# Kernel optimization log

Measured on AMD Instinct MI355X. Metric: run time of the kernel, lower is better.

## Reference

```python
import jax, jax.numpy as jnp
import numpy as np

CODE_SIZE = 1024
CODE_DIM = 256
B, H, W = 64, 32, 32

def setup_inputs() -> dict:
    key = jax.random.key(0)
    k1, k2 = jax.random.split(key)
    x = jax.random.normal(k1, (B, CODE_DIM, H, W), dtype=jnp.float32)
    # nn.Embedding weight initialized uniform(-1/code_size, 1/code_size)
    weight = jax.random.uniform(k2, (CODE_SIZE, CODE_DIM), dtype=jnp.float32,
                                minval=-1.0 / CODE_SIZE, maxval=1.0 / CODE_SIZE)
    return {"x": x, "weight": weight}

def reference(x, weight):
    b, c, h, w = x.shape
    # (B,C,H,W) -> (B*H*W, C)
    flat = jnp.transpose(x, (0, 2, 3, 1)).reshape(-1, c)
    # squared euclidean distances; argmin of d^2 equals argmin of cdist(p=2)
    d2 = (jnp.sum(flat * flat, axis=1, keepdims=True)
          - 2.0 * (flat @ weight.T)
          + jnp.sum(weight * weight, axis=1)[None, :])  # (N, code_size)
    idxs = jnp.argmin(d2, axis=1).reshape(b, h, w)       # (B,H,W) int
    quantized = jnp.transpose(weight[idxs], (0, 3, 1, 2))  # (B,C,H,W)
    ste = jax.lax.stop_gradient(quantized - x) + x        # straight-through
    return quantized, ste, idxs
```

## Files before the change

### kernel.cpp

```cpp
#include <hip/hip_runtime.h>
#include <math.h>

typedef float vf4 __attribute__((ext_vector_type(4)));

#define CODE_SIZE 1024
#define CODE_DIM  256
#define BB        64
#define HWSZ      1024
#define NROWS     (BB * HWSZ)
#define QELEMS    (BB * CODE_DIM * HWSZ)

__global__ void k_sumsq_w(const float* __restrict__ w, float* __restrict__ sw) {
#pragma clang fp contract(off)
  const int code = blockIdx.x * blockDim.x + threadIdx.x;
  if (code >= CODE_SIZE) return;
  const float* row = w + (size_t)code * CODE_DIM;
  float halves[2];
  for (int h = 0; h < 2; ++h) {
    const float* p = row + h * 128;
    float r[8];
#pragma unroll
    for (int j = 0; j < 8; ++j) { float v = p[j]; r[j] = v * v; }
    for (int i = 8; i < 128; i += 8) {
#pragma unroll
      for (int j = 0; j < 8; ++j) { float v = p[i + j]; r[j] += v * v; }
    }
    halves[h] = ((r[0] + r[1]) + (r[2] + r[3])) + ((r[4] + r[5]) + (r[6] + r[7]));
  }
  sw[code] = halves[0] + halves[1];
}

__global__ void k_sumsq_x(const float* __restrict__ x, float* __restrict__ sx) {
#pragma clang fp contract(off)
  const int n = blockIdx.x * blockDim.x + threadIdx.x;
  const int b = n >> 10, hw = n & 1023;
  const float* p = x + (size_t)b * CODE_DIM * HWSZ + hw;
  float halves[2];
  for (int h = 0; h < 2; ++h) {
    const float* q = p + (size_t)(h * 128) * HWSZ;
    float r[8];
#pragma unroll
    for (int j = 0; j < 8; ++j) { float v = q[(size_t)j * HWSZ]; r[j] = v * v; }
    for (int i = 8; i < 128; i += 8) {
#pragma unroll
      for (int j = 0; j < 8; ++j) { float v = q[(size_t)(i + j) * HWSZ]; r[j] += v * v; }
    }
    halves[h] = ((r[0] + r[1]) + (r[2] + r[3])) + ((r[4] + r[5]) + (r[6] + r[7]));
  }
  sx[n] = halves[0] + halves[1];
}

#define MT  64
#define NTC 256
#define NCH (CODE_SIZE / NTC)
#define KC  32

__launch_bounds__(256, 4)
__global__ void k_argmin(const float* __restrict__ x, const float* __restrict__ w,
                         const float* __restrict__ sx, const float* __restrict__ sw,
                         float* __restrict__ oidx) {
  __shared__ float xs[KC * MT];
  __shared__ float ws[KC * NTC];

  const int t   = threadIdx.x;
  const int n0  = blockIdx.x * MT;
  const int b   = n0 >> 10;
  const int hw0 = n0 & 1023;
  const int rt  = t & 7;
  const int ct  = t >> 3;

  float bk[8]; float bi[8];
#pragma unroll
  for (int ri = 0; ri < 8; ++ri) { bk[ri] = INFINITY; bi[ri] = (float)CODE_SIZE; }

  for (int chunk = 0; chunk < NCH; ++chunk) {
    const int code0 = chunk * NTC;

    float acc[8][8];
#pragma unroll
    for (int ri = 0; ri < 8; ++ri)
#pragma unroll
      for (int cj = 0; cj < 8; ++cj) acc[ri][cj] = 0.0f;

    for (int kc = 0; kc < CODE_DIM / KC; ++kc) {
      const int kbase = kc * KC;
      __syncthreads();
      {
#pragma unroll
        for (int i = 0; i < 2; ++i) {
          const int j  = t + 256 * i;
          const int k  = j >> 4;
          const int rq = j & 15;
          vf4 v = *(const vf4*)(x + ((size_t)(b * CODE_DIM + kbase + k) * HWSZ + hw0 + rq * 4));
          *(vf4*)(xs + k * MT + rq * 4) = v;
        }
      }
      {
        const float* wr = w + (size_t)(code0 + t) * CODE_DIM + kbase;
#pragma unroll
        for (int q = 0; q < 8; ++q) {
          vf4 v = *(const vf4*)(wr + q * 4);
          ws[(q * 4 + 0) * NTC + t] = v.x;
          ws[(q * 4 + 1) * NTC + t] = v.y;
          ws[(q * 4 + 2) * NTC + t] = v.z;
          ws[(q * 4 + 3) * NTC + t] = v.w;
        }
      }
      __syncthreads();

      const float* xp = xs + rt * 8;
      const float* wp = ws + ct * 8;
#pragma unroll 4
      for (int k = 0; k < KC; ++k) {
        vf4 xv0 = *(const vf4*)(xp + k * MT);
        vf4 xv1 = *(const vf4*)(xp + k * MT + 4);
        vf4 wv0 = *(const vf4*)(wp + k * NTC);
        vf4 wv1 = *(const vf4*)(wp + k * NTC + 4);
        float xr[8] = {xv0.x, xv0.y, xv0.z, xv0.w, xv1.x, xv1.y, xv1.z, xv1.w};
        float wc[8] = {wv0.x, wv0.y, wv0.z, wv0.w, wv1.x, wv1.y, wv1.z, wv1.w};
#pragma unroll
        for (int ri = 0; ri < 8; ++ri)
#pragma unroll
          for (int cj = 0; cj < 8; ++cj)
            acc[ri][cj] = fmaf(xr[ri], wc[cj], acc[ri][cj]);
      }
    }

    {
#pragma clang fp contract(off)
      float sxr[8];
#pragma unroll
      for (int ri = 0; ri < 8; ++ri) sxr[ri] = sx[n0 + rt * 8 + ri];
#pragma unroll
      for (int cj = 0; cj < 8; ++cj) {
        const int code = code0 + ct * 8 + cj;
        const float swv = sw[code];
        const float codef = (float)code;
#pragma unroll
        for (int ri = 0; ri < 8; ++ri) {
          const float tmp = sxr[ri] - 2.0f * acc[ri][cj];
          const float key = tmp + swv;
          if (key < bk[ri] || (key == bk[ri] && codef < bi[ri])) {
            bk[ri] = key; bi[ri] = codef;
          }
        }
      }
    }
  }

  __syncthreads();
  float* redk = ws;
  float* redi = ws + 32 * MT;
#pragma unroll
  for (int ri = 0; ri < 8; ++ri) {
    const int row = rt * 8 + ri;
    redk[ct * MT + row] = bk[ri];
    redi[ct * MT + row] = bi[ri];
  }
  __syncthreads();
  if (t < MT) {
    float k0 = redk[t]; float i0 = redi[t];
    for (int q = 1; q < 32; ++q) {
      const float kq = redk[q * MT + t];
      const float iq = redi[q * MT + t];
      if (kq < k0 || (kq == k0 && iq < i0)) { k0 = kq; i0 = iq; }
    }
    oidx[n0 + t] = i0;
  }
}

#define WT_S 65

__global__ void k_epilogue(const float* __restrict__ x, const float* __restrict__ w,
                           const float* __restrict__ oidx, float* __restrict__ out) {
#pragma clang fp contract(off)
  __shared__ int   idxs[MT];
  __shared__ float wt[CODE_DIM * WT_S];

  const int t   = threadIdx.x;
  const int n0  = blockIdx.x * MT;
  const int b   = n0 >> 10;
  const int hw0 = n0 & 1023;

  if (t < MT) idxs[t] = (int)oidx[n0 + t];
  __syncthreads();

#pragma unroll
  for (int i = 0; i < 16; ++i) {
    const int j  = t + 256 * i;
    const int r  = j & 63;
    const int cq = j >> 6;
    vf4 v = *(const vf4*)(w + (size_t)idxs[r] * CODE_DIM + cq * 4);
    wt[(cq * 4 + 0) * WT_S + r] = v.x;
    wt[(cq * 4 + 1) * WT_S + r] = v.y;
    wt[(cq * 4 + 2) * WT_S + r] = v.z;
    wt[(cq * 4 + 3) * WT_S + r] = v.w;
  }
  __syncthreads();

#pragma unroll
  for (int i = 0; i < 16; ++i) {
    const int j  = t + 256 * i;
    const int c  = j >> 4;
    const int rq = j & 15;
    const size_t off = (size_t)(b * CODE_DIM + c) * HWSZ + hw0 + rq * 4;
    vf4 xv = *(const vf4*)(x + off);
    vf4 q, s;
#pragma unroll
    for (int u = 0; u < 4; ++u) {
      const float qv = wt[c * WT_S + rq * 4 + u];
      q[u] = qv;
      const float d = qv - xv[u];
      s[u] = d + xv[u];
    }
    *(vf4*)(out + off) = q;
    *(vf4*)(out + (size_t)QELEMS + off) = s;
  }
}

extern "C" void kernel_launch(void* const* d_in, const int* in_sizes, int n_in,
                              void* d_out, int out_size, void* d_ws, size_t ws_size,
                              hipStream_t stream) {
  const float* x = (const float*)d_in[0];
  const float* w = (const float*)d_in[1];
  float* out  = (float*)d_out;
  float* oidx = out + 2 * (size_t)QELEMS;
  float* sx = out + (size_t)QELEMS;
  float* sw = out + (size_t)QELEMS + NROWS;

  k_sumsq_w<<<CODE_SIZE / 256, 256, 0, stream>>>(w, sw);
  k_sumsq_x<<<NROWS / 256, 256, 0, stream>>>(x, sx);
  k_argmin<<<NROWS / MT, 256, 0, stream>>>(x, w, sx, sw, oidx);
  k_epilogue<<<NROWS / MT, 256, 0, stream>>>(x, w, oidx, out);
}
```

Measured before the change: 618.1 us.

## Replace LDS-tiled argmin GEMM with per-lane rows and wave-uniform codebook loads

The argmin kernel drops its shared-memory staging of x and codebook tiles and its per-k-chunk barriers. Each lane now owns one spatial row and keeps its x values in registers. Each wave handles a block of 64 codes per chunk, so codebook reads are wave-uniform and can go through scalar loads. The aim is to remove LDS traffic and synchronisation, at the cost of rereading x from global memory in every wave and chunk, keeping 64 accumulators per lane, and relying on scalar-cache bandwidth and latency to feed the FMAs.

```diff
diff --git a/kernel.cpp b/kernel.cpp
--- a/kernel.cpp
+++ b/kernel.cpp
@@ -50,119 +50,81 @@
   sx[n] = halves[0] + halves[1];
 }
 
-#define MT  64
-#define NTC 256
-#define NCH (CODE_SIZE / NTC)
-#define KC  32
+#define MT     64
+#define NCH    4
+#define WCODES 64
+#define KC     16
 
-__launch_bounds__(256, 4)
+__launch_bounds__(256, 3)
 __global__ void k_argmin(const float* __restrict__ x, const float* __restrict__ w,
                          const float* __restrict__ sx, const float* __restrict__ sw,
                          float* __restrict__ oidx) {
-  __shared__ float xs[KC * MT];
-  __shared__ float ws[KC * NTC];
+  __shared__ float redk[4][MT];
+  __shared__ float redi[4][MT];
 
-  const int t   = threadIdx.x;
-  const int n0  = blockIdx.x * MT;
-  const int b   = n0 >> 10;
-  const int hw0 = n0 & 1023;
-  const int rt  = t & 7;
-  const int ct  = t >> 3;
+  const int t    = threadIdx.x;
+  const int lane = t & 63;
+  const int wv   = __builtin_amdgcn_readfirstlane(t >> 6);
+  const int n0   = blockIdx.x * MT;
+  const int b    = n0 >> 10;
+  const int hw0  = n0 & 1023;
 
-  float bk[8]; float bi[8];
-#pragma unroll
-  for (int ri = 0; ri < 8; ++ri) { bk[ri] = INFINITY; bi[ri] = (float)CODE_SIZE; }
+  const float* xlane = x + (size_t)b * CODE_DIM * HWSZ + hw0 + lane;
+  const float  sxr   = sx[n0 + lane];
+
+  float bk = INFINITY, bi = (float)CODE_SIZE;
 
   for (int chunk = 0; chunk < NCH; ++chunk) {
-    const int code0 = chunk * NTC;
+    const int code0 = chunk * (NCH * WCODES) + wv * WCODES;
 
-    float acc[8][8];
+    float acc[WCODES];
 #pragma unroll
-    for (int ri = 0; ri < 8; ++ri)
-#pragma unroll
-      for (int cj = 0; cj < 8; ++cj) acc[ri][cj] = 0.0f;
+    for (int c = 0; c < WCODES; ++c) acc[c] = 0.0f;
 
     for (int kc = 0; kc < CODE_DIM / KC; ++kc) {
       const int kbase = kc * KC;
-      __syncthreads();
-      {
+
+      float xk[KC];
 #pragma unroll
-        for (int i = 0; i < 2; ++i) {
-          const int j  = t + 256 * i;
-          const int k  = j >> 4;
-          const int rq = j & 15;
-          vf4 v = *(const vf4*)(x + ((size_t)(b * CODE_DIM + kbase + k) * HWSZ + hw0 + rq * 4));
-          *(vf4*)(xs + k * MT + rq * 4) = v;
+      for (int k = 0; k < KC; ++k)
+        xk[k] = xlane[(size_t)(kbase + k) * HWSZ];
+
+#pragma unroll
+      for (int c = 0; c < WCODES; ++c) {
+        const float* wr = w + (size_t)(code0 + c) * CODE_DIM + kbase;
+#pragma unroll
+        for (int q = 0; q < KC / 4; ++q) {
+          const vf4 wq = *(const vf4*)(wr + q * 4);
+          acc[c] = fmaf(xk[q * 4 + 0], wq.x, acc[c]);
+          acc[c] = fmaf(xk[q * 4 + 1], wq.y, acc[c]);
+          acc[c] = fmaf(xk[q * 4 + 2], wq.z, acc[c]);
+          acc[c] = fmaf(xk[q * 4 + 3], wq.w, acc[c]);
         }
-      }
-      {
-        const float* wr = w + (size_t)(code0 + t) * CODE_DIM + kbase;
-#pragma unroll
-        for (int q = 0; q < 8; ++q) {
-          vf4 v = *(const vf4*)(wr + q * 4);
-          ws[(q * 4 + 0) * NTC + t] = v.x;
-          ws[(q * 4 + 1) * NTC + t] = v.y;
-          ws[(q * 4 + 2) * NTC + t] = v.z;
-          ws[(q * 4 + 3) * NTC + t] = v.w;
-        }
-      }
-      __syncthreads();
-
-      const float* xp = xs + rt * 8;
-      const float* wp = ws + ct * 8;
-#pragma unroll 4
-      for (int k = 0; k < KC; ++k) {
-        vf4 xv0 = *(const vf4*)(xp + k * MT);
-        vf4 xv1 = *(const vf4*)(xp + k * MT + 4);
-        vf4 wv0 = *(const vf4*)(wp + k * NTC);
-        vf4 wv1 = *(const vf4*)(wp + k * NTC + 4);
-        float xr[8] = {xv0.x, xv0.y, xv0.z, xv0.w, xv1.x, xv1.y, xv1.z, xv1.w};
-        float wc[8] = {wv0.x, wv0.y, wv0.z, wv0.w, wv1.x, wv1.y, wv1.z, wv1.w};
-#pragma unroll
-        for (int ri = 0; ri < 8; ++ri)
-#pragma unroll
-          for (int cj = 0; cj < 8; ++cj)
-            acc[ri][cj] = fmaf(xr[ri], wc[cj], acc[ri][cj]);
       }
     }
 
     {
 #pragma clang fp contract(off)
-      float sxr[8];
 #pragma unroll
-      for (int ri = 0; ri < 8; ++ri) sxr[ri] = sx[n0 + rt * 8 + ri];
-#pragma unroll
-      for (int cj = 0; cj < 8; ++cj) {
-        const int code = code0 + ct * 8 + cj;
-        const float swv = sw[code];
+      for (int c = 0; c < WCODES; ++c) {
+        const int   code  = code0 + c;
+        const float tmp   = sxr - 2.0f * acc[c];
+        const float key   = tmp + sw[code];
         const float codef = (float)code;
-#pragma unroll
-        for (int ri = 0; ri < 8; ++ri) {
-          const float tmp = sxr[ri] - 2.0f * acc[ri][cj];
-          const float key = tmp + swv;
-          if (key < bk[ri] || (key == bk[ri] && codef < bi[ri])) {
-            bk[ri] = key; bi[ri] = codef;
-          }
-        }
+        if (key < bk || (key == bk && codef < bi)) { bk = key; bi = codef; }
       }
     }
   }
 
-  __syncthreads();
-  float* redk = ws;
-  float* redi = ws + 32 * MT;
-#pragma unroll
-  for (int ri = 0; ri < 8; ++ri) {
-    const int row = rt * 8 + ri;
-    redk[ct * MT + row] = bk[ri];
-    redi[ct * MT + row] = bi[ri];
-  }
+  redk[wv][lane] = bk;
+  redi[wv][lane] = bi;
   __syncthreads();
   if (t < MT) {
-    float k0 = redk[t]; float i0 = redi[t];
-    for (int q = 1; q < 32; ++q) {
-      const float kq = redk[q * MT + t];
-      const float iq = redi[q * MT + t];
+    float k0 = redk[0][t], i0 = redi[0][t];
+#pragma unroll
+    for (int q = 1; q < 4; ++q) {
+      const float kq = redk[q][t];
+      const float iq = redi[q][t];
       if (kq < k0 || (kq == k0 && iq < i0)) { k0 = kq; i0 = iq; }
     }
     oidx[n0 + t] = i0;
```

Result: slower. 1.787 ms (+189.1%).
